# Performance work log

Hardware: AMD Instinct MI355X
Metric: run time of the kernel (lower is better)

The kernel has to match this reference:

```python
import jax, jax.numpy as jnp
import numpy as np

EPS = 0.0  # init eps


def setup_inputs() -> dict:
    key = jax.random.key(0)
    k1, k2 = jax.random.split(key)
    features = jax.random.normal(k1, (8, 64, 100000), dtype=jnp.float32)
    coords = jax.random.normal(k2, (8, 3, 100000), dtype=jnp.float32)
    return {"features": features, "coords": coords, "resolution": 32}


def _voxelize(features, coords, r):
    # coords: [B, 3, N], features: [B, C, N]
    coords = jax.lax.stop_gradient(coords)  # original does coords.detach()
    norm_coords = coords - jnp.mean(coords, axis=2, keepdims=True)
    # normalize=True branch: divide by 2*max point radius, shift to [0,1]
    radius = jnp.linalg.norm(norm_coords, axis=1, keepdims=True)        # [B,1,N]
    scale = jnp.max(radius, axis=2, keepdims=True) * 2.0 + EPS          # [B,1,1]
    norm_coords = norm_coords / scale + 0.5
    norm_coords = jnp.clip(norm_coords * r, 0, r - 1)                   # [B,3,N]
    vox = jnp.round(norm_coords).astype(jnp.int32)                      # [B,3,N]

    B, C, N = features.shape
    flat_idx = (vox[:, 0] * r + vox[:, 1]) * r + vox[:, 2]              # [B,N]
    seg_ids = (flat_idx + jnp.arange(B, dtype=jnp.int32)[:, None] * (r ** 3)).reshape(-1)

    feats = jnp.transpose(features, (0, 2, 1)).reshape(B * N, C)        # [B*N,C]
    sums = jax.ops.segment_sum(feats, seg_ids, num_segments=B * r ** 3)  # [B*r^3,C]
    cnts = jax.ops.segment_sum(jnp.ones((B * N,), features.dtype), seg_ids,
                               num_segments=B * r ** 3)                  # [B*r^3]
    avg = sums / jnp.maximum(cnts, 1.0)[:, None]
    vox_feat = jnp.transpose(avg.reshape(B, r ** 3, C), (0, 2, 1)).reshape(B, C, r, r, r)
    return vox_feat, norm_coords


def reference(features, coords, resolution):
    return _voxelize(features, coords, int(resolution))
```

## Files before the change

### kernel.cpp

```cpp
#include <hip/hip_runtime.h>
#include <math.h>

static constexpr int B = 8;
static constexpr int C = 64;
static constexpr int N = 100000;
static constexpr int RES = 32;
static constexpr int R3 = RES * RES * RES;
static constexpr int NQ = N / 4;

static constexpr int   SCALE_BITS = 19;
static constexpr float FSCALE     = (float)(1 << SCALE_BITS);
static constexpr float INV_FSCALE = 1.0f / FSCALE;

static constexpr size_t MEAN_OFF = 0;
static constexpr size_t MAX_OFF  = 192;
static constexpr size_t CNT_OFF  = 256;
static constexpr size_t VID_OFF  = CNT_OFF + (size_t)B * R3 * sizeof(int);
static constexpr size_t HDR_BYTES = 256;

__device__ __forceinline__ int vhash(int v) { return v ^ (v >> 5) ^ (v >> 10); }

__device__ __forceinline__ double block_reduce_sum(double v) {
    for (int off = 32; off > 0; off >>= 1) v += __shfl_down(v, off, 64);
    __shared__ double s[4];
    int lane = threadIdx.x & 63, w = threadIdx.x >> 6;
    if (lane == 0) s[w] = v;
    __syncthreads();
    if (threadIdx.x == 0) v = (s[0] + s[1]) + (s[2] + s[3]);
    return v;
}

__device__ __forceinline__ float block_reduce_max(float v) {
    for (int off = 32; off > 0; off >>= 1) v = fmaxf(v, __shfl_down(v, off, 64));
    __shared__ float s[4];
    int lane = threadIdx.x & 63, w = threadIdx.x >> 6;
    if (lane == 0) s[w] = v;
    __syncthreads();
    if (threadIdx.x == 0) v = fmaxf(fmaxf(s[0], s[1]), fmaxf(s[2], s[3]));
    return v;
}

__global__ void k_mean(const float* __restrict__ coords, double* __restrict__ mean_sum,
                       int* __restrict__ cnt) {
    int gtid = blockIdx.x * blockDim.x + threadIdx.x;
    int4* c4 = (int4*)cnt;
    for (int i = gtid; i < B * R3 / 4; i += gridDim.x * blockDim.x)
        c4[i] = make_int4(0, 0, 0, 0);

    const int NSLICE = 8;
    int pair  = blockIdx.x % (B * 3);
    int slice = blockIdx.x / (B * 3);
    const float* p = coords + (size_t)pair * N;
    double acc = 0.0;
#pragma unroll 4
    for (int i = slice * 256 + threadIdx.x; i < N; i += NSLICE * 256)
        acc += (double)p[i];
    acc = block_reduce_sum(acc);
    if (threadIdx.x == 0) atomicAdd(&mean_sum[pair], acc);
}

__global__ void k_max(const float* __restrict__ coords,
                      const double* __restrict__ mean_sum,
                      unsigned int* __restrict__ maxr2) {
    const int NSLICE = 16;
    int b     = blockIdx.x % B;
    int slice = blockIdx.x / B;
    __shared__ float sm[3];
    if (threadIdx.x < 3)
        sm[threadIdx.x] = (float)(mean_sum[b * 3 + threadIdx.x] / (double)N);
    __syncthreads();
    float mx = sm[0], my = sm[1], mz = sm[2];
    const float4* px = (const float4*)(coords + (size_t)(b * 3 + 0) * N);
    const float4* py = (const float4*)(coords + (size_t)(b * 3 + 1) * N);
    const float4* pz = (const float4*)(coords + (size_t)(b * 3 + 2) * N);
    float m = 0.0f;
    for (int i = slice * 256 + threadIdx.x; i < NQ; i += NSLICE * 256) {
        float4 x4 = px[i], y4 = py[i], z4 = pz[i];
        float x, y, z;
        x = x4.x - mx; y = y4.x - my; z = z4.x - mz; m = fmaxf(m, x*x + y*y + z*z);
        x = x4.y - mx; y = y4.y - my; z = z4.y - mz; m = fmaxf(m, x*x + y*y + z*z);
        x = x4.z - mx; y = y4.z - my; z = z4.z - mz; m = fmaxf(m, x*x + y*y + z*z);
        x = x4.w - mx; y = y4.w - my; z = z4.w - mz; m = fmaxf(m, x*x + y*y + z*z);
    }
    m = block_reduce_max(m);
    if (threadIdx.x == 0) atomicMax(&maxr2[b], __float_as_uint(m));
}

__global__ __launch_bounds__(256) void k_vid(const float* __restrict__ coords,
                      const double* __restrict__ mean_sum,
                      const unsigned int* __restrict__ maxr2,
                      unsigned short* __restrict__ vid,
                      float* __restrict__ out_norm,
                      int* __restrict__ cnt) {
    int b = blockIdx.y;
    __shared__ float sm[4];
    if (threadIdx.x < 3)
        sm[threadIdx.x] = (float)(mean_sum[b * 3 + threadIdx.x] / (double)N);
    if (threadIdx.x == 3)
        sm[3] = 2.0f * sqrtf(__uint_as_float(maxr2[b]));
    __syncthreads();
    int q = blockIdx.x * 256 + threadIdx.x;
    if (q >= NQ) return;
    float m0 = sm[0], m1 = sm[1], m2 = sm[2], scale = sm[3];

    const float4* p0 = (const float4*)(coords + (size_t)(b * 3 + 0) * N);
    const float4* p1 = (const float4*)(coords + (size_t)(b * 3 + 1) * N);
    const float4* p2 = (const float4*)(coords + (size_t)(b * 3 + 2) * N);
    float4* o0 = (float4*)(out_norm + (size_t)(b * 3 + 0) * N);
    float4* o1 = (float4*)(out_norm + (size_t)(b * 3 + 1) * N);
    float4* o2 = (float4*)(out_norm + (size_t)(b * 3 + 2) * N);
    float4 x4 = p0[q], y4 = p1[q], z4 = p2[q];

#define NORM1(v, mm) { v = (v - mm) / scale + 0.5f; v = v * (float)RES;     \
                       v = fminf(fmaxf(v, 0.0f), (float)(RES - 1)); }
    NORM1(x4.x, m0); NORM1(x4.y, m0); NORM1(x4.z, m0); NORM1(x4.w, m0);
    NORM1(y4.x, m1); NORM1(y4.y, m1); NORM1(y4.z, m1); NORM1(y4.w, m1);
    NORM1(z4.x, m2); NORM1(z4.y, m2); NORM1(z4.z, m2); NORM1(z4.w, m2);
#undef NORM1
    o0[q] = x4; o1[q] = y4; o2[q] = z4;

    int* cb = cnt + (size_t)b * R3;
    int f0 = ((int)rintf(x4.x) * RES + (int)rintf(y4.x)) * RES + (int)rintf(z4.x);
    int f1 = ((int)rintf(x4.y) * RES + (int)rintf(y4.y)) * RES + (int)rintf(z4.y);
    int f2 = ((int)rintf(x4.z) * RES + (int)rintf(y4.z)) * RES + (int)rintf(z4.z);
    int f3 = ((int)rintf(x4.w) * RES + (int)rintf(y4.w)) * RES + (int)rintf(z4.w);
    ushort4 h;
    h.x = (unsigned short)vhash(f0); h.y = (unsigned short)vhash(f1);
    h.z = (unsigned short)vhash(f2); h.w = (unsigned short)vhash(f3);
    ((ushort4*)(vid + (size_t)b * N))[q] = h;
    atomicAdd(&cb[f0], 1); atomicAdd(&cb[f1], 1);
    atomicAdd(&cb[f2], 1); atomicAdd(&cb[f3], 1);
}

__global__ __launch_bounds__(1024) void k_accum(const unsigned short* __restrict__ vid,
                                                const float* __restrict__ feats,
                                                const int* __restrict__ cnt,
                                                float* __restrict__ out_vox) {
    extern __shared__ char smem[];
    int* grid = (int*)smem;
    constexpr int BS = 1024, U = 4, STEP = BS * U;
    constexpr int NITER = NQ / STEP;
    constexpr int NMAIN = NITER * STEP;
    int b = blockIdx.x & 7;
    int c = blockIdx.x >> 3;
    int4* g4 = (int4*)grid;
    for (int i = threadIdx.x; i < R3 / 4; i += BS) g4[i] = make_int4(0, 0, 0, 0);
    __syncthreads();
    const uint2*  vp = (const uint2*)(vid + (size_t)b * N);
    const float4* fp = (const float4*)(feats + ((size_t)(b * C + c)) * N);
    const int tid = threadIdx.x;

    uint2 v0[U], v1[U]; float4 f0[U], f1[U];

#define LOADC(dstv, dstf, chunk)                                            \
    {   int _base = (chunk) * STEP + tid;                                   \
        _Pragma("unroll")                                                   \
        for (int u = 0; u < U; ++u) { dstv[u] = vp[_base + u * BS];         \
                                      dstf[u] = fp[_base + u * BS]; } }
#define PROC(sv, sf)                                                        \
    {   _Pragma("unroll")                                                   \
        for (int u = 0; u < U; ++u) {                                       \
            uint2 vv = sv[u]; float4 ff = sf[u];                            \
            atomicAdd(&grid[(int)(vv.x & 0xffffu)], __float2int_rn(ff.x * FSCALE)); \
            atomicAdd(&grid[(int)(vv.x >> 16)],     __float2int_rn(ff.y * FSCALE)); \
            atomicAdd(&grid[(int)(vv.y & 0xffffu)], __float2int_rn(ff.z * FSCALE)); \
            atomicAdd(&grid[(int)(vv.y >> 16)],     __float2int_rn(ff.w * FSCALE)); \
        } }

    LOADC(v0, f0, 0);
    for (int it = 0; it < NITER; it += 2) {
        int c1 = (it + 1 < NITER) ? it + 1 : NITER - 1;
        LOADC(v1, f1, c1);
        __builtin_amdgcn_sched_barrier(0);
        PROC(v0, f0);
        int c2 = (it + 2 < NITER) ? it + 2 : NITER - 1;
        LOADC(v0, f0, c2);
        __builtin_amdgcn_sched_barrier(0);
        PROC(v1, f1);
    }
#undef LOADC
#undef PROC
    for (int i = NMAIN + tid; i < NQ; i += BS) {
        uint2 v = vp[i]; float4 f = fp[i];
        atomicAdd(&grid[(int)(v.x & 0xffffu)], __float2int_rn(f.x * FSCALE));
        atomicAdd(&grid[(int)(v.x >> 16)],     __float2int_rn(f.y * FSCALE));
        atomicAdd(&grid[(int)(v.y & 0xffffu)], __float2int_rn(f.z * FSCALE));
        atomicAdd(&grid[(int)(v.y >> 16)],     __float2int_rn(f.w * FSCALE));
    }
    __syncthreads();
    const int* cp = cnt + (size_t)b * R3;
    float* op = out_vox + ((size_t)(b * C + c)) * R3;
    for (int i = threadIdx.x; i < R3; i += BS) {
        float s = (float)grid[vhash(i)] * INV_FSCALE;
        op[i] = s / fmaxf((float)cp[i], 1.0f);
    }
}

extern "C" void kernel_launch(void* const* d_in, const int* in_sizes, int n_in,
                              void* d_out, int out_size, void* d_ws, size_t ws_size,
                              hipStream_t stream) {
    const float* feats  = (const float*)d_in[0];
    const float* coords = (const float*)d_in[1];
    float* out_vox  = (float*)d_out;
    float* out_norm = out_vox + (size_t)B * C * R3;

    double*         mean_sum = (double*)((char*)d_ws + MEAN_OFF);
    unsigned int*   maxr2    = (unsigned int*)((char*)d_ws + MAX_OFF);
    int*            cnt      = (int*)((char*)d_ws + CNT_OFF);
    unsigned short* vid      = (unsigned short*)((char*)d_ws + VID_OFF);

    static bool attr_done = false;
    if (!attr_done) {
        hipFuncSetAttribute((const void*)k_accum,
                            hipFuncAttributeMaxDynamicSharedMemorySize, R3 * sizeof(int));
        attr_done = true;
    }

    hipMemsetAsync(d_ws, 0, HDR_BYTES, stream);

    k_mean<<<B * 3 * 8, 256, 0, stream>>>(coords, mean_sum, cnt);
    k_max<<<B * 16, 256, 0, stream>>>(coords, mean_sum, maxr2);
    k_vid<<<dim3((NQ + 255) / 256, B), 256, 0, stream>>>(coords, mean_sum, maxr2, vid, out_norm, cnt);
    k_accum<<<B * C, 1024, R3 * sizeof(int), stream>>>(vid, feats, cnt, out_vox);
}
```

Measured before the change: 375.3 us.

## Prefetch feature chunks before zeroing shared grid, unroll fully with nontemporal loads

Restructures the accumulation kernel so the first two chunks of vids and features are loaded before the shared-memory histogram is zeroed, hiding global-memory latency behind the clear. The chunk loop becomes a fully unrolled four-chunk schedule with U=6, and feature loads use nontemporal hints to avoid polluting cache. The final normalization pass is vectorized to int4 count reads and float4 stores, and the launch bound gains a min-blocks hint. Register pressure from the larger unroll and the occupancy hint could cause spills.

```diff
diff --git a/kernel.cpp b/kernel.cpp
--- a/kernel.cpp
+++ b/kernel.cpp
@@ -11,6 +11,8 @@
 static constexpr int   SCALE_BITS = 19;
 static constexpr float FSCALE     = (float)(1 << SCALE_BITS);
 static constexpr float INV_FSCALE = 1.0f / FSCALE;
+
+typedef float vfloat4 __attribute__((ext_vector_type(4)));
 
 static constexpr size_t MEAN_OFF = 0;
 static constexpr size_t MAX_OFF  = 192;
@@ -132,67 +134,80 @@
     atomicAdd(&cb[f2], 1); atomicAdd(&cb[f3], 1);
 }
 
-__global__ __launch_bounds__(1024) void k_accum(const unsigned short* __restrict__ vid,
-                                                const float* __restrict__ feats,
-                                                const int* __restrict__ cnt,
-                                                float* __restrict__ out_vox) {
+__global__ __launch_bounds__(1024, 4) void k_accum(const unsigned short* __restrict__ vid,
+                                                   const float* __restrict__ feats,
+                                                   const int* __restrict__ cnt,
+                                                   float* __restrict__ out_vox) {
     extern __shared__ char smem[];
     int* grid = (int*)smem;
-    constexpr int BS = 1024, U = 4, STEP = BS * U;
-    constexpr int NITER = NQ / STEP;
+    constexpr int BS = 1024, U = 6, STEP = BS * U;
+    constexpr int NITER = 4;
     constexpr int NMAIN = NITER * STEP;
     int b = blockIdx.x & 7;
     int c = blockIdx.x >> 3;
-    int4* g4 = (int4*)grid;
-    for (int i = threadIdx.x; i < R3 / 4; i += BS) g4[i] = make_int4(0, 0, 0, 0);
-    __syncthreads();
-    const uint2*  vp = (const uint2*)(vid + (size_t)b * N);
-    const float4* fp = (const float4*)(feats + ((size_t)(b * C + c)) * N);
+    const uint2*   vp = (const uint2*)(vid + (size_t)b * N);
+    const vfloat4* fp = (const vfloat4*)(feats + ((size_t)(b * C + c)) * N);
     const int tid = threadIdx.x;
 
-    uint2 v0[U], v1[U]; float4 f0[U], f1[U];
+    uint2 vA[U], vB[U]; vfloat4 fA[U], fB[U];
 
 #define LOADC(dstv, dstf, chunk)                                            \
     {   int _base = (chunk) * STEP + tid;                                   \
         _Pragma("unroll")                                                   \
-        for (int u = 0; u < U; ++u) { dstv[u] = vp[_base + u * BS];         \
-                                      dstf[u] = fp[_base + u * BS]; } }
+        for (int u = 0; u < U; ++u) {                                       \
+            dstv[u] = vp[_base + u * BS];                                   \
+            dstf[u] = __builtin_nontemporal_load(&fp[_base + u * BS]);      \
+        } }
 #define PROC(sv, sf)                                                        \
     {   _Pragma("unroll")                                                   \
         for (int u = 0; u < U; ++u) {                                       \
-            uint2 vv = sv[u]; float4 ff = sf[u];                            \
+            uint2 vv = sv[u]; vfloat4 ff = sf[u];                           \
             atomicAdd(&grid[(int)(vv.x & 0xffffu)], __float2int_rn(ff.x * FSCALE)); \
             atomicAdd(&grid[(int)(vv.x >> 16)],     __float2int_rn(ff.y * FSCALE)); \
             atomicAdd(&grid[(int)(vv.y & 0xffffu)], __float2int_rn(ff.z * FSCALE)); \
             atomicAdd(&grid[(int)(vv.y >> 16)],     __float2int_rn(ff.w * FSCALE)); \
         } }
 
-    LOADC(v0, f0, 0);
-    for (int it = 0; it < NITER; it += 2) {
-        int c1 = (it + 1 < NITER) ? it + 1 : NITER - 1;
-        LOADC(v1, f1, c1);
-        __builtin_amdgcn_sched_barrier(0);
-        PROC(v0, f0);
-        int c2 = (it + 2 < NITER) ? it + 2 : NITER - 1;
-        LOADC(v0, f0, c2);
-        __builtin_amdgcn_sched_barrier(0);
-        PROC(v1, f1);
-    }
+    LOADC(vA, fA, 0);
+    LOADC(vB, fB, 1);
+    int4* g4 = (int4*)grid;
+    for (int i = tid; i < R3 / 4; i += BS) g4[i] = make_int4(0, 0, 0, 0);
+    __syncthreads();
+
+    __builtin_amdgcn_sched_barrier(0);
+    PROC(vA, fA);
+    LOADC(vA, fA, 2);
+    __builtin_amdgcn_sched_barrier(0);
+    PROC(vB, fB);
+    LOADC(vB, fB, 3);
+    __builtin_amdgcn_sched_barrier(0);
+    PROC(vA, fA);
+    __builtin_amdgcn_sched_barrier(0);
+    PROC(vB, fB);
 #undef LOADC
 #undef PROC
+
     for (int i = NMAIN + tid; i < NQ; i += BS) {
-        uint2 v = vp[i]; float4 f = fp[i];
+        uint2 v = vp[i];
+        vfloat4 f = __builtin_nontemporal_load(&fp[i]);
         atomicAdd(&grid[(int)(v.x & 0xffffu)], __float2int_rn(f.x * FSCALE));
         atomicAdd(&grid[(int)(v.x >> 16)],     __float2int_rn(f.y * FSCALE));
         atomicAdd(&grid[(int)(v.y & 0xffffu)], __float2int_rn(f.z * FSCALE));
         atomicAdd(&grid[(int)(v.y >> 16)],     __float2int_rn(f.w * FSCALE));
     }
     __syncthreads();
-    const int* cp = cnt + (size_t)b * R3;
-    float* op = out_vox + ((size_t)(b * C + c)) * R3;
-    for (int i = threadIdx.x; i < R3; i += BS) {
-        float s = (float)grid[vhash(i)] * INV_FSCALE;
-        op[i] = s / fmaxf((float)cp[i], 1.0f);
+
+    const int4* cp4 = (const int4*)(cnt + (size_t)b * R3);
+    float4* op4 = (float4*)(out_vox + ((size_t)(b * C + c)) * R3);
+    for (int i = tid; i < R3 / 4; i += BS) {
+        int4 c4v = cp4[i];
+        int base = i * 4;
+        float4 o;
+        o.x = ((float)grid[vhash(base + 0)] * INV_FSCALE) / fmaxf((float)c4v.x, 1.0f);
+        o.y = ((float)grid[vhash(base + 1)] * INV_FSCALE) / fmaxf((float)c4v.y, 1.0f);
+        o.z = ((float)grid[vhash(base + 2)] * INV_FSCALE) / fmaxf((float)c4v.z, 1.0f);
+        o.w = ((float)grid[vhash(base + 3)] * INV_FSCALE) / fmaxf((float)c4v.w, 1.0f);
+        op4[i] = o;
     }
 }
 
@@ -211,12 +226,12 @@
 
     static bool attr_done = false;
     if (!attr_done) {
-        hipFuncSetAttribute((const void*)k_accum,
+        (void)hipFuncSetAttribute((const void*)k_accum,
                             hipFuncAttributeMaxDynamicSharedMemorySize, R3 * sizeof(int));
         attr_done = true;
     }
 
-    hipMemsetAsync(d_ws, 0, HDR_BYTES, stream);
+    (void)hipMemsetAsync(d_ws, 0, HDR_BYTES, stream);
 
     k_mean<<<B * 3 * 8, 256, 0, stream>>>(coords, mean_sum, cnt);
     k_max<<<B * 16, 256, 0, stream>>>(coords, mean_sum, maxr2);
```

Result: faster. 357.0 us (-4.9%).
